# Performance work log

Hardware: AMD Instinct MI355X
Metric: run time of the kernel (lower is better)

Reference implementation:

```python
import jax, jax.numpy as jnp
import numpy as np


def setup_inputs() -> dict:
    key = jax.random.key(0)
    k1, k2, k3, k4 = jax.random.split(key, 4)
    TOKENS, IN_F, OUT_F = 4096, 4096, 11008
    x = jax.random.normal(k1, (TOKENS, IN_F), dtype=jnp.float32)
    # int8-valued weights stored in fp32 buffer, as in the torch module
    quantized_weight = jax.random.randint(k2, (OUT_F, IN_F), -128, 128).astype(jnp.float32)
    # per-output-channel scales, positive, small (like max|w|/127)
    weight_scales = (jax.random.uniform(k3, (OUT_F, 1), dtype=jnp.float32) * 0.03 + 0.001)
    bias = jax.random.normal(k4, (OUT_F,), dtype=jnp.float32)
    return {"x": x, "quantized_weight": quantized_weight,
            "weight_scales": weight_scales, "bias": bias}


def reference(x, quantized_weight, weight_scales, bias):
    # dequantize: per-channel scale broadcast over in_features
    weight = quantized_weight * weight_scales  # [out, in]
    # F.linear: x @ weight.T + bias
    return jnp.dot(x, weight.T) + bias
```

## Files before the change

kernel.cpp:

```cpp
#include <hip/hip_runtime.h>
#include <hip/hip_bf16.h>


typedef __attribute__((ext_vector_type(4))) int   i32x4;
typedef __attribute__((ext_vector_type(4))) float f32x4;
typedef __attribute__((ext_vector_type(4))) unsigned int u32x4;

__device__ static inline unsigned int pack4(int q0, int q1, int q2, int q3) {
    return (unsigned)(q0 & 255) | ((unsigned)(q1 & 255) << 8) |
           ((unsigned)(q2 & 255) << 16) | ((unsigned)(q3 & 255) << 24);
}

__global__ void w_to_i8(const float* __restrict__ in,
                        u32x4* __restrict__ out, long n16) {
    const long stride = (long)gridDim.x * blockDim.x;
    for (long i = (long)blockIdx.x * blockDim.x + threadIdx.x; i < n16; i += stride) {
        const f32x4* p = reinterpret_cast<const f32x4*>(in) + i * 4;
        u32x4 o;
#pragma unroll
        for (int v = 0; v < 4; ++v) {
            f32x4 f = p[v];
            o[v] = pack4(__float2int_rn(f[0]), __float2int_rn(f[1]),
                         __float2int_rn(f[2]), __float2int_rn(f[3]));
        }
        out[i] = o;
    }
}

__global__ void x_quant_i8(const float* __restrict__ x,
                           unsigned int* __restrict__ xq,
                           float* __restrict__ sx, int K) {
    const int row = blockIdx.x;
    const int tid = threadIdx.x;
    const float* xr = x + (size_t)row * K;
    float m = 0.f;
    for (int b = tid * 16; b < K; b += blockDim.x * 16) {
        const f32x4* p = (const f32x4*)(xr + b);
#pragma unroll
        for (int v = 0; v < 4; ++v) {
            f32x4 f = p[v];
            m = fmaxf(m, fmaxf(fmaxf(fabsf(f[0]), fabsf(f[1])),
                               fmaxf(fabsf(f[2]), fabsf(f[3]))));
        }
    }
#pragma unroll
    for (int off = 32; off; off >>= 1) m = fmaxf(m, __shfl_xor(m, off));
    __shared__ float red[8];
    if ((tid & 63) == 0) red[tid >> 6] = m;
    __syncthreads();
    const int nw = blockDim.x >> 6;
    m = red[0];
    for (int i = 1; i < nw; ++i) m = fmaxf(m, red[i]);
    const float inv = (m > 0.f) ? 127.0f / m : 0.f;
    if (tid == 0) sx[row] = m * (1.0f / 127.0f);
    for (int b = tid * 16; b < K; b += blockDim.x * 16) {
        const f32x4* p = (const f32x4*)(xr + b);
        u32x4 o;
#pragma unroll
        for (int v = 0; v < 4; ++v) {
            f32x4 f = p[v];
            int q0 = min(127, max(-127, __float2int_rn(f[0] * inv)));
            int q1 = min(127, max(-127, __float2int_rn(f[1] * inv)));
            int q2 = min(127, max(-127, __float2int_rn(f[2] * inv)));
            int q3 = min(127, max(-127, __float2int_rn(f[3] * inv)));
            o[v] = pack4(q0, q1, q2, q3);
        }
        *reinterpret_cast<u32x4*>((char*)xq + (size_t)row * K + b) = o;
    }
}


#define GLOAD16(src, dst) __builtin_amdgcn_global_load_lds( \
    (const __attribute__((address_space(1))) void*)(src),   \
    (__attribute__((address_space(3))) void*)(dst), 16, 0, 0)

#define FENCE() asm volatile("" ::: "memory")
#define BAR()  do { FENCE(); __builtin_amdgcn_s_barrier(); FENCE(); } while (0)
#define WAIT_VM(n) asm volatile("s_waitcnt vmcnt(" #n ")" ::: "memory")
#define WAIT_LGKM0() asm volatile("s_waitcnt lgkmcnt(0)" ::: "memory")
#define SCHED0() __builtin_amdgcn_sched_barrier(0)

__global__ __launch_bounds__(512, 2)
void qlinear_gemm_i8p8(const char* __restrict__ A,
                       const char* __restrict__ B,
                       const float* __restrict__ sx,
                       const float* __restrict__ scales,
                       const float* __restrict__ bias,
                       float* __restrict__ C,
                       int M, int N, int K, int nbx) {
    __shared__ __align__(128) char smem[98304];

    const int tid  = threadIdx.x;
    const int lane = tid & 63;
    const int wid  = tid >> 6;
    const int wr   = wid >> 2;
    const int wc   = wid & 3;

    const int nwg = gridDim.x;
    const int q = nwg >> 3, r = nwg & 7;
    const int xcd = blockIdx.x & 7, boff_ = blockIdx.x >> 3;
    const int swz = (xcd < r ? xcd * (q + 1) : r * (q + 1) + (xcd - r) * q) + boff_;
    const int bcol = swz % nbx;
    const int brow = swz / nbx;

    const char* Ag = A + (size_t)brow * 256 * K;
    const char* Bg = B + (size_t)bcol * 256 * K;

    const int srow = tid >> 2;
    const size_t gsrc = ((size_t)srow * K) + (((tid & 3) ^ ((tid >> 3) & 3)) << 4);
    const int ldst = tid * 16;

    auto stageH = [&](int mat, int h, int rs, int t) {
        const char* G = (mat ? Bg : Ag) + (size_t)h * 128 * K;
        GLOAD16(G + gsrc + (size_t)t * 64,
                smem + mat * 49152 + rs * 16384 + h * 8192 + ldst);
    };

    const int cph  = ((lane >> 4) ^ ((lane >> 1) & 3)) << 4;
    const int arow = (wr * 128 + (lane & 15)) * 64 + cph;
    const int brow_ = (wc * 64 + (lane & 15)) * 64 + cph;

    i32x4 acc[8][4] = {};
    i32x4 a0[4], a1[4], b0[2], b1[2];

    auto rdA = [&](int rg, int mh, i32x4 (&d)[4]) {
        const char* p = smem + rg * 16384 + arow + mh * 4096;
#pragma unroll
        for (int i = 0; i < 4; ++i) d[i] = *(const i32x4*)(p + i * 1024);
    };
    auto rdB = [&](int rg, int nh, i32x4 (&d)[2]) {
        const char* p = smem + 49152 + rg * 16384 + brow_ + nh * 2048;
#pragma unroll
        for (int n = 0; n < 2; ++n) d[n] = *(const i32x4*)(p + n * 1024);
    };
    auto mfma8 = [&](const i32x4 (&a)[4], const i32x4 (&b)[2], int qm, int qn) {
        __builtin_amdgcn_s_setprio(1);
#pragma unroll
        for (int i = 0; i < 4; ++i)
#pragma unroll
            for (int n = 0; n < 2; ++n)
                acc[qm * 4 + i][qn * 2 + n] = __builtin_amdgcn_mfma_i32_16x16x64_i8(
                    a[i], b[n], acc[qm * 4 + i][qn * 2 + n], 0, 0, 0);
        __builtin_amdgcn_s_setprio(0);
    };

    const int NT = K / 64;

    stageH(0, 0, 0, 0); stageH(1, 0, 0, 0); stageH(0, 1, 0, 0); stageH(1, 1, 0, 0);
    stageH(0, 0, 1, 1); stageH(1, 0, 1, 1); stageH(0, 1, 1, 1); stageH(1, 1, 1, 1);
    WAIT_VM(4); BAR();

    int rg = 0;
    for (int t = 0; t < NT - 2; ++t) {
        int rs = rg + 2; if (rs >= 3) rs -= 3;
        rdA(rg, 0, a0); rdB(rg, 0, b0);
        stageH(0, 0, rs, t + 2);
        BAR(); WAIT_LGKM0(); SCHED0();
        mfma8(a0, b0, 0, 0);
        BAR();
        rdA(rg, 1, a1);
        stageH(1, 0, rs, t + 2);
        BAR(); WAIT_LGKM0(); SCHED0();
        mfma8(a1, b0, 1, 0);
        BAR();
        rdB(rg, 1, b1);
        stageH(0, 1, rs, t + 2);
        BAR(); WAIT_LGKM0(); SCHED0();
        mfma8(a0, b1, 0, 1);
        BAR();
        stageH(1, 1, rs, t + 2);
        mfma8(a1, b1, 1, 1);
        WAIT_VM(4);
        BAR();
        rg = (rg == 2) ? 0 : rg + 1;
    }
    rdA(rg, 0, a0); rdB(rg, 0, b0);
    BAR(); WAIT_LGKM0(); SCHED0();
    mfma8(a0, b0, 0, 0);
    BAR();
    rdA(rg, 1, a1);
    BAR(); WAIT_LGKM0(); SCHED0();
    mfma8(a1, b0, 1, 0);
    BAR();
    rdB(rg, 1, b1);
    BAR(); WAIT_LGKM0(); SCHED0();
    mfma8(a0, b1, 0, 1);
    BAR();
    mfma8(a1, b1, 1, 1);
    WAIT_VM(0);
    BAR();
    rg = (rg == 2) ? 0 : rg + 1;
    rdA(rg, 0, a0); rdB(rg, 0, b0);
    WAIT_LGKM0(); SCHED0();
    mfma8(a0, b0, 0, 0);
    rdA(rg, 1, a1);
    WAIT_LGKM0(); SCHED0();
    mfma8(a1, b0, 1, 0);
    rdB(rg, 1, b1);
    WAIT_LGKM0(); SCHED0();
    mfma8(a0, b1, 0, 1);
    mfma8(a1, b1, 1, 1);

    const int lc  = lane & 15;
    const int lr4 = (lane >> 4) * 4;
    float sarr[4], barr[4];
#pragma unroll
    for (int ni = 0; ni < 4; ++ni) {
        const int n = bcol * 256 + wc * 64 + (ni >> 1) * 32 + (ni & 1) * 16 + lc;
        sarr[ni] = scales[n];
        barr[ni] = bias[n];
    }
#pragma unroll
    for (int mi = 0; mi < 8; ++mi) {
        const int mb = brow * 256 + wr * 128 + (mi >> 2) * 64 + (mi & 3) * 16 + lr4;
#pragma unroll
        for (int j = 0; j < 4; ++j) {
            const size_t rowoff = (size_t)(mb + j) * N;
            const float sm = sx[mb + j];
#pragma unroll
            for (int ni = 0; ni < 4; ++ni) {
                const int n = bcol * 256 + wc * 64 + (ni >> 1) * 32 + (ni & 1) * 16 + lc;
                C[rowoff + n] = fmaf((float)acc[mi][ni][j], sm * sarr[ni], barr[ni]);
            }
        }
    }
}

__global__ void qlinear_fallback(const float* __restrict__ A,
                                 const float* __restrict__ B,
                                 const float* __restrict__ scales,
                                 const float* __restrict__ bias,
                                 float* __restrict__ C, int M, int N, int K) {
    __shared__ float As[16][17], Bs[16][17];
    const int tx = threadIdx.x, ty = threadIdx.y;
    const int row = blockIdx.y * 16 + ty;
    const int col = blockIdx.x * 16 + tx;
    float acc = 0.f;
    for (int k0 = 0; k0 < K; k0 += 16) {
        As[ty][tx] = A[(long)row * K + k0 + tx];
        Bs[ty][tx] = B[(long)(blockIdx.x * 16 + ty) * K + k0 + tx];
        __syncthreads();
#pragma unroll
        for (int kk = 0; kk < 16; ++kk) acc += As[ty][kk] * Bs[tx][kk];
        __syncthreads();
    }
    C[(long)row * N + col] = fmaf(acc, scales[col], bias[col]);
}

extern "C" void kernel_launch(void* const* d_in, const int* in_sizes, int n_in,
                              void* d_out, int out_size, void* d_ws, size_t ws_size,
                              hipStream_t stream) {
    const float* x      = (const float*)d_in[0];
    const float* w      = (const float*)d_in[1];
    const float* scales = (const float*)d_in[2];
    const float* bias   = (const float*)d_in[3];
    float* out = (float*)d_out;

    const int N = in_sizes[2];
    const int K = (int)((long)in_sizes[1] / N);
    const int M = (int)((long)in_sizes[0] / K);

    const size_t need = (size_t)M * K + (size_t)N * K + (size_t)M * 4;
    const bool ok = (ws_size >= need) && (M % 256) == 0 && (N % 256) == 0 &&
                    (K % 64) == 0 && (K / 64) >= 4 && (K % 16) == 0;

    if (ok) {
        char* xq = (char*)d_ws;
        char* wq = xq + (size_t)M * K;
        float* sxbuf = (float*)(wq + (size_t)N * K);

        x_quant_i8<<<M, 256, 0, stream>>>(x, (unsigned int*)xq, sxbuf, K);
        w_to_i8<<<2048, 256, 0, stream>>>(w, (u32x4*)wq, (long)N * K / 16);

        const int nbx = N / 256;
        const int nwg = (M / 256) * nbx;
        qlinear_gemm_i8p8<<<nwg, 512, 0, stream>>>(xq, wq, sxbuf, scales, bias,
                                                   out, M, N, K, nbx);
    } else {
        dim3 grid(N / 16, M / 16), blk(16, 16);
        qlinear_fallback<<<grid, blk, 0, stream>>>(x, w, scales, bias, out, M, N, K);
    }
}
```

Measured before the change: 266.2 us.

## Double K tile to 128 with two-stage LDS ring and staggered prefetch

Restructures the int8 GEMM main loop to consume a K-depth of 128 per iteration instead of 64. LDS staging moves from a triple-buffered 64-byte-wide ring to a double-buffered 128-byte-wide layout with a new XOR swizzle, and loads for the next tile are staggered across the compute phases. Each barrier-separated phase now issues twice as many MFMAs, meant to amortise barrier and sync overhead per unit of work. LDS use grows to 128 KB per block, which may limit occupancy to one block per CU despite launch bounds requesting two, and a shallower ring may expose more load latency.

```diff
diff --git a/kernel.cpp b/kernel.cpp
--- a/kernel.cpp
+++ b/kernel.cpp
@@ -78,17 +78,18 @@
 #define BAR()  do { FENCE(); __builtin_amdgcn_s_barrier(); FENCE(); } while (0)
 #define WAIT_VM(n) asm volatile("s_waitcnt vmcnt(" #n ")" ::: "memory")
 #define WAIT_LGKM0() asm volatile("s_waitcnt lgkmcnt(0)" ::: "memory")
+#define PACE_LGKM(n) asm volatile("s_waitcnt lgkmcnt(" #n ")" ::: "memory")
 #define SCHED0() __builtin_amdgcn_sched_barrier(0)
 
 __global__ __launch_bounds__(512, 2)
-void qlinear_gemm_i8p8(const char* __restrict__ A,
-                       const char* __restrict__ B,
-                       const float* __restrict__ sx,
-                       const float* __restrict__ scales,
-                       const float* __restrict__ bias,
-                       float* __restrict__ C,
-                       int M, int N, int K, int nbx) {
-    __shared__ __align__(128) char smem[98304];
+void qlinear_gemm_i8k128(const char* __restrict__ A,
+                         const char* __restrict__ B,
+                         const float* __restrict__ sx,
+                         const float* __restrict__ scales,
+                         const float* __restrict__ bias,
+                         float* __restrict__ C,
+                         int M, int N, int K, int nbx) {
+    __shared__ __align__(128) char smem[131072];
 
     const int tid  = threadIdx.x;
     const int lane = tid & 63;
@@ -106,100 +107,129 @@
     const char* Ag = A + (size_t)brow * 256 * K;
     const char* Bg = B + (size_t)bcol * 256 * K;
 
-    const int srow = tid >> 2;
-    const size_t gsrc = ((size_t)srow * K) + (((tid & 3) ^ ((tid >> 3) & 3)) << 4);
-    const int ldst = tid * 16;
-
-    auto stageH = [&](int mat, int h, int rs, int t) {
-        const char* G = (mat ? Bg : Ag) + (size_t)h * 128 * K;
-        GLOAD16(G + gsrc + (size_t)t * 64,
-                smem + mat * 49152 + rs * 16384 + h * 8192 + ldst);
-    };
-
-    const int cph  = ((lane >> 4) ^ ((lane >> 1) & 3)) << 4;
-    const int arow = (wr * 128 + (lane & 15)) * 64 + cph;
-    const int brow_ = (wc * 64 + (lane & 15)) * 64 + cph;
+    size_t sA[2], sB[2];
+#pragma unroll
+    for (int g = 0; g < 2; ++g) {
+        const int c = tid + g * 512, rl = c >> 3, j = c & 7;
+        const int rowA = ((rl >> 6) << 7) + (rl & 63);
+        const int rowB = ((rl >> 5) << 6) + (rl & 31);
+        sA[g] = (size_t)rowA * K + ((j ^ (rl & 7)) << 4);
+        sB[g] = (size_t)rowB * K + ((j ^ (rl & 7)) << 4);
+    }
+    const int ld0 = tid * 16;
+
+    auto stageA = [&](int rg, int h, int t) {
+        const char* G = Ag + (size_t)h * 64 * K + (size_t)t * 128;
+        char* base = smem + rg * 32768 + h * 16384;
+        GLOAD16(G + sA[0], base + ld0);
+        GLOAD16(G + sA[1], base + ld0 + 8192);
+    };
+    auto stageB = [&](int rg, int h, int t) {
+        const char* G = Bg + (size_t)h * 32 * K + (size_t)t * 128;
+        char* base = smem + 65536 + rg * 32768 + h * 16384;
+        GLOAD16(G + sB[0], base + ld0);
+        GLOAD16(G + sB[1], base + ld0 + 8192);
+    };
+
+    const int px0 = (((lane >> 4) ^ (lane & 7)) << 4);
+    const int px1 = (((4 + (lane >> 4)) ^ (lane & 7)) << 4);
+    const int arow = (wr * 64 + (lane & 15)) * 128;
+    const int brw  = (wc * 32 + (lane & 15)) * 128;
 
     i32x4 acc[8][4] = {};
-    i32x4 a0[4], a1[4], b0[2], b1[2];
-
-    auto rdA = [&](int rg, int mh, i32x4 (&d)[4]) {
-        const char* p = smem + rg * 16384 + arow + mh * 4096;
-#pragma unroll
-        for (int i = 0; i < 4; ++i) d[i] = *(const i32x4*)(p + i * 1024);
-    };
-    auto rdB = [&](int rg, int nh, i32x4 (&d)[2]) {
-        const char* p = smem + 49152 + rg * 16384 + brow_ + nh * 2048;
-#pragma unroll
-        for (int n = 0; n < 2; ++n) d[n] = *(const i32x4*)(p + n * 1024);
-    };
-    auto mfma8 = [&](const i32x4 (&a)[4], const i32x4 (&b)[2], int qm, int qn) {
+    i32x4 a0[8], a1[8], b0[4], b1[4];
+
+    auto rdA = [&](int rg, int mh, i32x4 (&d)[8]) {
+        const char* p = smem + rg * 32768 + mh * 16384 + arow;
+#pragma unroll
+        for (int i = 0; i < 4; ++i) {
+            d[i * 2]     = *(const i32x4*)(p + i * 2048 + px0);
+            d[i * 2 + 1] = *(const i32x4*)(p + i * 2048 + px1);
+        }
+    };
+    auto rdB = [&](int rg, int nh, i32x4 (&d)[4]) {
+        const char* p = smem + 65536 + rg * 32768 + nh * 16384 + brw;
+#pragma unroll
+        for (int n = 0; n < 2; ++n) {
+            d[n * 2]     = *(const i32x4*)(p + n * 2048 + px0);
+            d[n * 2 + 1] = *(const i32x4*)(p + n * 2048 + px1);
+        }
+    };
+    auto mfma16 = [&](const i32x4 (&a)[8], const i32x4 (&b)[4], int mh, int nh) {
         __builtin_amdgcn_s_setprio(1);
 #pragma unroll
         for (int i = 0; i < 4; ++i)
 #pragma unroll
-            for (int n = 0; n < 2; ++n)
-                acc[qm * 4 + i][qn * 2 + n] = __builtin_amdgcn_mfma_i32_16x16x64_i8(
-                    a[i], b[n], acc[qm * 4 + i][qn * 2 + n], 0, 0, 0);
+            for (int n = 0; n < 2; ++n) {
+                i32x4& ac = acc[mh * 4 + i][nh * 2 + n];
+                ac = __builtin_amdgcn_mfma_i32_16x16x64_i8(a[i * 2], b[n * 2], ac, 0, 0, 0);
+                ac = __builtin_amdgcn_mfma_i32_16x16x64_i8(a[i * 2 + 1], b[n * 2 + 1], ac, 0, 0, 0);
+            }
         __builtin_amdgcn_s_setprio(0);
     };
 
-    const int NT = K / 64;
-
-    stageH(0, 0, 0, 0); stageH(1, 0, 0, 0); stageH(0, 1, 0, 0); stageH(1, 1, 0, 0);
-    stageH(0, 0, 1, 1); stageH(1, 0, 1, 1); stageH(0, 1, 1, 1); stageH(1, 1, 1, 1);
-    WAIT_VM(4); BAR();
-
-    int rg = 0;
+    const int NT = K / 128;
+
+    stageA(0, 0, 0); stageB(0, 0, 0); stageA(0, 1, 0); stageB(0, 1, 0);
+    stageA(1, 0, 1); stageB(1, 0, 1); stageA(1, 1, 1);
+    WAIT_VM(6); BAR();
+
     for (int t = 0; t < NT - 2; ++t) {
-        int rs = rg + 2; if (rs >= 3) rs -= 3;
-        rdA(rg, 0, a0); rdB(rg, 0, b0);
-        stageH(0, 0, rs, t + 2);
-        BAR(); WAIT_LGKM0(); SCHED0();
-        mfma8(a0, b0, 0, 0);
-        BAR();
-        rdA(rg, 1, a1);
-        stageH(1, 0, rs, t + 2);
-        BAR(); WAIT_LGKM0(); SCHED0();
-        mfma8(a1, b0, 1, 0);
-        BAR();
-        rdB(rg, 1, b1);
-        stageH(0, 1, rs, t + 2);
-        BAR(); WAIT_LGKM0(); SCHED0();
-        mfma8(a0, b1, 0, 1);
-        BAR();
-        stageH(1, 1, rs, t + 2);
-        mfma8(a1, b1, 1, 1);
-        WAIT_VM(4);
-        BAR();
-        rg = (rg == 2) ? 0 : rg + 1;
-    }
-    rdA(rg, 0, a0); rdB(rg, 0, b0);
-    BAR(); WAIT_LGKM0(); SCHED0();
-    mfma8(a0, b0, 0, 0);
-    BAR();
-    rdA(rg, 1, a1);
-    BAR(); WAIT_LGKM0(); SCHED0();
-    mfma8(a1, b0, 1, 0);
-    BAR();
-    rdB(rg, 1, b1);
-    BAR(); WAIT_LGKM0(); SCHED0();
-    mfma8(a0, b1, 0, 1);
-    BAR();
-    mfma8(a1, b1, 1, 1);
-    WAIT_VM(0);
-    BAR();
-    rg = (rg == 2) ? 0 : rg + 1;
-    rdA(rg, 0, a0); rdB(rg, 0, b0);
-    WAIT_LGKM0(); SCHED0();
-    mfma8(a0, b0, 0, 0);
-    rdA(rg, 1, a1);
-    WAIT_LGKM0(); SCHED0();
-    mfma8(a1, b0, 1, 0);
-    rdB(rg, 1, b1);
-    WAIT_LGKM0(); SCHED0();
-    mfma8(a0, b1, 0, 1);
-    mfma8(a1, b1, 1, 1);
+        const int c = t & 1, o = c ^ 1;
+        rdA(c, 0, a0); rdB(c, 0, b0);
+        stageB(o, 1, t + 1);
+        PACE_LGKM(8);
+        BAR(); WAIT_LGKM0(); SCHED0();
+        mfma16(a0, b0, 0, 0);
+        BAR();
+        rdA(c, 1, a1);
+        stageA(c, 0, t + 2);
+        BAR(); WAIT_LGKM0(); SCHED0();
+        mfma16(a1, b0, 1, 0);
+        BAR();
+        rdB(c, 1, b1);
+        stageB(c, 0, t + 2);
+        BAR(); WAIT_LGKM0(); SCHED0();
+        mfma16(a0, b1, 0, 1);
+        BAR();
+        stageA(c, 1, t + 2);
+        mfma16(a1, b1, 1, 1);
+        WAIT_VM(6);
+        BAR();
+    }
+    {
+        const int c = (NT - 2) & 1, o = c ^ 1;
+        rdA(c, 0, a0); rdB(c, 0, b0);
+        stageB(o, 1, NT - 1);
+        PACE_LGKM(8);
+        BAR(); WAIT_LGKM0(); SCHED0();
+        mfma16(a0, b0, 0, 0);
+        BAR();
+        rdA(c, 1, a1);
+        BAR(); WAIT_LGKM0(); SCHED0();
+        mfma16(a1, b0, 1, 0);
+        BAR();
+        rdB(c, 1, b1);
+        BAR(); WAIT_LGKM0(); SCHED0();
+        mfma16(a0, b1, 0, 1);
+        BAR();
+        mfma16(a1, b1, 1, 1);
+        WAIT_VM(0);
+        BAR();
+    }
+    {
+        const int c = (NT - 1) & 1;
+        rdA(c, 0, a0); rdB(c, 0, b0);
+        WAIT_LGKM0(); SCHED0();
+        mfma16(a0, b0, 0, 0);
+        rdA(c, 1, a1);
+        WAIT_LGKM0(); SCHED0();
+        mfma16(a1, b0, 1, 0);
+        rdB(c, 1, b1);
+        WAIT_LGKM0(); SCHED0();
+        mfma16(a0, b1, 0, 1);
+        mfma16(a1, b1, 1, 1);
+    }
 
     const int lc  = lane & 15;
     const int lr4 = (lane >> 4) * 4;
@@ -262,7 +292,7 @@
 
     const size_t need = (size_t)M * K + (size_t)N * K + (size_t)M * 4;
     const bool ok = (ws_size >= need) && (M % 256) == 0 && (N % 256) == 0 &&
-                    (K % 64) == 0 && (K / 64) >= 4 && (K % 16) == 0;
+                    (K % 128) == 0 && (K / 128) >= 3 && (K % 16) == 0;
 
     if (ok) {
         char* xq = (char*)d_ws;
@@ -274,8 +304,8 @@
 
         const int nbx = N / 256;
         const int nwg = (M / 256) * nbx;
-        qlinear_gemm_i8p8<<<nwg, 512, 0, stream>>>(xq, wq, sxbuf, scales, bias,
-                                                   out, M, N, K, nbx);
+        qlinear_gemm_i8k128<<<nwg, 512, 0, stream>>>(xq, wq, sxbuf, scales, bias,
+                                                     out, M, N, K, nbx);
     } else {
         dim3 grid(N / 16, M / 16), blk(16, 16);
         qlinear_fallback<<<grid, blk, 0, stream>>>(x, w, scales, bias, out, M, N, K);
```

Measured after the change: 253.8 us. 4.7% less time.
